# Kernel tuning notes

Measured on AMD Instinct MI355X. Metric: run time of the kernel, lower is better.

## Reference

```python
import jax, jax.numpy as jnp
import numpy as np

L = 2048          # seq len
DIM = 1024        # model dim
NL = 12           # num layers
VOCAB = 50257
PAD_VOCAB = 50264 # vocab padded to multiple of 8 for embedding
N = 16            # ssm state dim
K = 4             # conv kernel size
E = 2048          # d_inner = expand * dim
DTR = 64          # dt_rank = ceil(dim/16)
EPS = 1e-5


def setup_inputs() -> dict:
    key = jax.random.key(0)
    ks = jax.random.split(key, 12)
    s = 0.02
    f32 = jnp.float32
    # HiPPO-style A init: A_log = log(1..N) broadcast over channels
    A_log = jnp.log(jnp.broadcast_to(jnp.arange(1, N + 1, dtype=f32), (NL, E, N)))
    return {
        "input_ids": jax.random.randint(ks[0], (L,), 0, VOCAB),
        "embed": jax.random.normal(ks[1], (PAD_VOCAB, DIM), f32) * s,
        "in_proj_w": jax.random.normal(ks[2], (NL, 2 * E, DIM), f32) * s,
        "conv_w": jax.random.normal(ks[3], (NL, E, K), f32) * s,
        "conv_b": jnp.zeros((NL, E), f32),
        "x_proj_w": jax.random.normal(ks[4], (NL, DTR + 2 * N, E), f32) * s,
        "dt_proj_w": jax.random.normal(ks[5], (NL, E, DTR), f32) * s,
        "dt_proj_b": jax.random.normal(ks[6], (NL, E), f32) * 0.1,
        "A_log": A_log,
        "D_param": jnp.ones((NL, E), f32),
        "out_proj_w": jax.random.normal(ks[7], (NL, DIM, E), f32) * s,
        "norm_w": jnp.ones((NL, DIM), f32),
        "norm_f_w": jnp.ones((DIM,), f32),
        "head_w": jax.random.normal(ks[8], (VOCAB, DIM), f32) * s,
    }


def rmsnorm(x, w):
    # per-token RMSNorm over last axis (matches eqx.nn.RMSNorm vmapped per token)
    inv = jax.lax.rsqrt(jnp.mean(x * x, axis=-1, keepdims=True) + EPS)
    return x * inv * w


def causal_dw_conv(x, w, b):
    # x: [L, E], w: [E, K] depthwise causal conv, b: [E]
    out = jax.lax.conv_general_dilated(
        x.T[None],            # [1, E, L]
        w[:, None, :],        # [E, 1, K]
        (1,), [(K - 1, 0)],
        feature_group_count=E,
        dimension_numbers=("NCH", "OIH", "NCH"),
    )
    return out[0].T + b       # [L, E]


def mamba_block(x, in_w, cw, cb, xp_w, dt_w, dt_b, A_log, D, out_w):
    # x: [L, DIM]
    xz = x @ in_w.T                       # [L, 2E]
    xi, z = xz[:, :E], xz[:, E:]
    xc = jax.nn.silu(causal_dw_conv(xi, cw, cb))   # [L, E]
    dbc = xc @ xp_w.T                     # [L, DTR + 2N]
    dt = jax.nn.softplus(dbc[:, :DTR] @ dt_w.T + dt_b)  # [L, E]
    B = dbc[:, DTR:DTR + N]               # [L, N]
    C = dbc[:, DTR + N:]                  # [L, N]
    A = -jnp.exp(A_log)                   # [E, N]
    dA = jnp.exp(dt[:, :, None] * A)                       # [L, E, N]
    dBu = dt[:, :, None] * B[:, None, :] * xc[:, :, None]  # [L, E, N]

    def step(h, inp):
        dA_t, dBu_t = inp
        h = dA_t * h + dBu_t
        return h, h

    _, hs = jax.lax.scan(step, jnp.zeros((E, N), x.dtype), (dA, dBu))
    y = jnp.einsum("len,ln->le", hs, C) + D * xc
    y = y * jax.nn.silu(z)
    return y @ out_w.T                    # [L, DIM]


def reference(input_ids, embed, in_proj_w, conv_w, conv_b, x_proj_w,
              dt_proj_w, dt_proj_b, A_log, D_param, out_proj_w,
              norm_w, norm_f_w, head_w):
    x = embed[input_ids]                  # [L, DIM]
    res = None
    for i in range(NL):
        res = x + res if res is not None else x
        h = rmsnorm(res, norm_w[i])
        x = mamba_block(h, in_proj_w[i], conv_w[i], conv_b[i], x_proj_w[i],
                        dt_proj_w[i], dt_proj_b[i], A_log[i], D_param[i],
                        out_proj_w[i])
    res = x + res
    x = rmsnorm(res, norm_f_w)
    return x @ head_w.T                   # [L, VOCAB]
```

## Files before the change

kernel.cpp:

```cpp
#include <hip/hip_runtime.h>
#include <math.h>

#define LSEQ 2048
#define DMODEL 1024
#define NLAYER 12
#define NVOCAB 50257
#define NPADV 50304
#define EDIM 2048
#define NST 16
#define DTRANK 64
#define EPSV 1e-5f
#define NCHUNK 64
#define TCHUNK 32

typedef __attribute__((ext_vector_type(4))) float float4v;
typedef __attribute__((ext_vector_type(8))) short short8v;
typedef __attribute__((ext_vector_type(4))) unsigned short ushort4v;
typedef unsigned short u16;

__device__ __forceinline__ u16 f2bf(float f) {
    union { float f; unsigned int u; } v; v.f = f;
    unsigned int r = v.u + 0x7FFFu + ((v.u >> 16) & 1u);
    return (u16)(r >> 16);
}

__device__ __forceinline__ ushort4v cvt4(float4 a) {
    ushort4v r; r[0] = f2bf(a.x); r[1] = f2bf(a.y); r[2] = f2bf(a.z); r[3] = f2bf(a.w);
    return r;
}

__device__ __forceinline__ short8v pack8(float4 a, float4 b) {
    short8v r;
    r[0] = (short)f2bf(a.x); r[1] = (short)f2bf(a.y); r[2] = (short)f2bf(a.z); r[3] = (short)f2bf(a.w);
    r[4] = (short)f2bf(b.x); r[5] = (short)f2bf(b.y); r[6] = (short)f2bf(b.z); r[7] = (short)f2bf(b.w);
    return r;
}

__device__ __forceinline__ float4v mfma_bf16(short8v a, short8v b, float4v c) {
    return __builtin_amdgcn_mfma_f32_16x16x32_bf16(a, b, c, 0, 0, 0);
}

__device__ __forceinline__ void gload_lds16(const void* g, void* l) {
    __builtin_amdgcn_global_load_lds(
        (const __attribute__((address_space(1))) unsigned int*)g,
        (__attribute__((address_space(3))) unsigned int*)l,
        16, 0, 0);
}

__global__ __launch_bounds__(256) void k_embed(const int* __restrict__ ids,
                                               const float* __restrict__ emb,
                                               float* __restrict__ res) {
    const int t = blockIdx.x;
    const int row = ids[t];
    ((float4*)(res + (size_t)t * DMODEL))[threadIdx.x] =
        ((const float4*)(emb + (size_t)row * DMODEL))[threadIdx.x];
}

template<bool ADD>
__global__ __launch_bounds__(256) void k_addnorm(float* __restrict__ res,
                                                 const float* __restrict__ xin,
                                                 const float* __restrict__ w,
                                                 u16* __restrict__ h) {
    const int t = blockIdx.x;
    const int i = threadIdx.x;
    float4 r = ((float4*)(res + (size_t)t * DMODEL))[i];
    if (ADD) {
        float4 xv = ((const float4*)(xin + (size_t)t * DMODEL))[i];
        r.x += xv.x; r.y += xv.y; r.z += xv.z; r.w += xv.w;
        ((float4*)(res + (size_t)t * DMODEL))[i] = r;
    }
    float ss = r.x * r.x + r.y * r.y + r.z * r.z + r.w * r.w;
#pragma unroll
    for (int off = 32; off > 0; off >>= 1) ss += __shfl_xor(ss, off);
    __shared__ float part[4];
    if ((i & 63) == 0) part[i >> 6] = ss;
    __syncthreads();
    float tot = part[0] + part[1] + part[2] + part[3];
    const float inv = rsqrtf(tot * (1.f / DMODEL) + EPSV);
    float4 wv = ((const float4*)w)[i];
    float4 o;
    o.x = r.x * inv * wv.x; o.y = r.y * inv * wv.y;
    o.z = r.z * inv * wv.z; o.w = r.w * inv * wv.w;
    ((ushort4v*)(h + (size_t)t * DMODEL))[i] = cvt4(o);
}

__global__ __launch_bounds__(256) void k_cvt(const float* __restrict__ s, u16* __restrict__ d,
                                             long long n, long long ntot) {
    const long long stride = (long long)gridDim.x * 256 * 8;
    for (long long i = ((long long)blockIdx.x * 256 + threadIdx.x) * 8; i < ntot; i += stride) {
        ushort4v lo, hi;
        if (i < n) {
            float4 a = *(const float4*)(s + i);
            float4 b = *(const float4*)(s + i + 4);
            lo = cvt4(a); hi = cvt4(b);
        } else {
            lo[0] = lo[1] = lo[2] = lo[3] = 0;
            hi[0] = hi[1] = hi[2] = hi[3] = 0;
        }
        *(ushort4v*)(d + i) = lo;
        *(ushort4v*)(d + i + 4) = hi;
    }
}

__global__ __launch_bounds__(256) void k_cvt2(const float* __restrict__ sa, u16* __restrict__ da, long long na,
                                              const float* __restrict__ sb, u16* __restrict__ db, long long nb) {
    const long long tot = na + nb;
    const long long stride = (long long)gridDim.x * 256 * 8;
    for (long long i = ((long long)blockIdx.x * 256 + threadIdx.x) * 8; i < tot; i += stride) {
        const float* s; u16* d; long long o;
        if (i < na) { s = sa; d = da; o = i; } else { s = sb; d = db; o = i - na; }
        float4 a = *(const float4*)(s + o);
        float4 b = *(const float4*)(s + o + 4);
        *(ushort4v*)(d + o) = cvt4(a);
        *(ushort4v*)(d + o + 4) = cvt4(b);
    }
}

template<int TM, int TN>
__global__ __launch_bounds__(256) void k_gemm_bf(const u16* __restrict__ A,
                                                 const u16* __restrict__ W,
                                                 float* __restrict__ C,
                                                 int N, int K, int ldc) {
    constexpr int NI = TM / 32, NJ = TN / 32, CA = TM / 64, CB = TN / 64;
    __shared__ u16 As[TM * 32];
    __shared__ u16 Bs[TN * 32];
    const int tid = threadIdx.x;
    const int lane = tid & 63;
    const int wave = tid >> 6;
    const int l16 = lane & 15;
    const int quad = lane >> 4;
    const int wm = (wave >> 1) * (TM / 2);
    const int wn = (wave & 1) * (TN / 2);
    const int srow = lane >> 2;
    const int scol = (lane & 3) * 8;
    const int bm = blockIdx.x, bn = blockIdx.y;

    const u16* Ab = A + ((size_t)bm * TM + srow) * K + scol;
    const u16* Wb = W + ((size_t)bn * TN + srow) * K + scol;

    float4v acc[NI][NJ];
#pragma unroll
    for (int i = 0; i < NI; ++i)
#pragma unroll
        for (int j = 0; j < NJ; ++j)
#pragma unroll
            for (int r = 0; r < 4; ++r) acc[i][j][r] = 0.f;

    for (int k0 = 0; k0 < K; k0 += 32) {
#pragma unroll
        for (int c = 0; c < CA; ++c) {
            const int chunk = wave * CA + c;
            gload_lds16(Ab + (size_t)chunk * 16 * K + k0, &As[chunk * 512]);
        }
#pragma unroll
        for (int c = 0; c < CB; ++c) {
            const int chunk = wave * CB + c;
            gload_lds16(Wb + (size_t)chunk * 16 * K + k0, &Bs[chunk * 512]);
        }
        __syncthreads();
        short8v af[NI], bfr[NJ];
#pragma unroll
        for (int i = 0; i < NI; ++i)
            af[i] = *(const short8v*)&As[(wm + i * 16 + l16) * 32 + quad * 8];
#pragma unroll
        for (int j = 0; j < NJ; ++j)
            bfr[j] = *(const short8v*)&Bs[(wn + j * 16 + l16) * 32 + quad * 8];
#pragma unroll
        for (int i = 0; i < NI; ++i)
#pragma unroll
            for (int j = 0; j < NJ; ++j)
                acc[i][j] = mfma_bf16(af[i], bfr[j], acc[i][j]);
        __syncthreads();
    }

#pragma unroll
    for (int i = 0; i < NI; ++i) {
        const int row0 = bm * TM + wm + i * 16 + quad * 4;
#pragma unroll
        for (int j = 0; j < NJ; ++j) {
            const int col = bn * TN + wn + j * 16 + l16;
            if (col < N) {
#pragma unroll
                for (int r = 0; r < 4; ++r)
                    C[(size_t)(row0 + r) * ldc + col] = acc[i][j][r];
            }
        }
    }
}

template<int EPI>
__global__ __launch_bounds__(256) void k_gemm(const float* __restrict__ A,
                                              const float* __restrict__ W,
                                              float* __restrict__ C,
                                              const float* __restrict__ bias,
                                              int N, int K, int lda, int ldw, int ldc) {
    __shared__ u16 As[128][32];
    __shared__ u16 Bs[128][32];
    const int tid = threadIdx.x;
    const int lane = tid & 63;
    const int wave = tid >> 6;
    const int l16 = lane & 15;
    const int quad = lane >> 4;
    const int wm = (wave >> 1) * 64;
    const int wn = (wave & 1) * 64;
    const int srow = tid >> 3;
    const int scol = (tid & 7) * 4;
    const int bm = blockIdx.x, bn = blockIdx.y;

    const float* Ap = A + (size_t)(bm * 128 + srow) * lda + scol;
    const int gn0 = bn * 128 + srow;

    float4 apf[4], bpf[4];
#pragma unroll
    for (int i = 0; i < 4; ++i) {
        apf[i] = *(const float4*)(Ap + (size_t)(32 * i) * lda);
        const int gn = gn0 + 32 * i;
        bpf[i] = (gn < N) ? *(const float4*)(W + (size_t)gn * ldw + scol)
                          : make_float4(0.f, 0.f, 0.f, 0.f);
    }

    float4v acc[4][4];
#pragma unroll
    for (int i = 0; i < 4; ++i)
#pragma unroll
        for (int j = 0; j < 4; ++j)
#pragma unroll
            for (int r = 0; r < 4; ++r) acc[i][j][r] = 0.f;

    int k0 = 0;
    while (true) {
#pragma unroll
        for (int i = 0; i < 4; ++i) {
            *(ushort4v*)&As[srow + 32 * i][scol] = cvt4(apf[i]);
            *(ushort4v*)&Bs[srow + 32 * i][scol] = cvt4(bpf[i]);
        }
        __syncthreads();
        k0 += 32;
        const bool more = (k0 < K);
        if (more) {
#pragma unroll
            for (int i = 0; i < 4; ++i) {
                apf[i] = *(const float4*)(Ap + (size_t)(32 * i) * lda + k0);
                const int gn = gn0 + 32 * i;
                bpf[i] = (gn < N) ? *(const float4*)(W + (size_t)gn * ldw + scol + k0)
                                  : make_float4(0.f, 0.f, 0.f, 0.f);
            }
        }
        short8v af[4], bfr[4];
#pragma unroll
        for (int i = 0; i < 4; ++i)
            af[i] = *(const short8v*)&As[wm + i * 16 + l16][quad * 8];
#pragma unroll
        for (int j = 0; j < 4; ++j)
            bfr[j] = *(const short8v*)&Bs[wn + j * 16 + l16][quad * 8];
#pragma unroll
        for (int i = 0; i < 4; ++i)
#pragma unroll
            for (int j = 0; j < 4; ++j)
                acc[i][j] = mfma_bf16(af[i], bfr[j], acc[i][j]);
        if (!more) break;
        __syncthreads();
    }

#pragma unroll
    for (int i = 0; i < 4; ++i) {
        const int row0 = bm * 128 + wm + i * 16 + quad * 4;
#pragma unroll
        for (int j = 0; j < 4; ++j) {
            const int col = bn * 128 + wn + j * 16 + l16;
            if (col < N) {
#pragma unroll
                for (int r = 0; r < 4; ++r) {
                    float v = acc[i][j][r];
                    if (EPI == 1) {
                        v += bias[col];
                        v = (v > 20.f) ? v : log1pf(__expf(v));
                    }
                    C[(size_t)(row0 + r) * ldc + col] = v;
                }
            }
        }
    }
}

__global__ __launch_bounds__(256) void k_conv(const float* __restrict__ xz,
                                              const float* __restrict__ cw,
                                              const float* __restrict__ cb,
                                              float* __restrict__ xc) {
    const int e = blockIdx.x * 256 + threadIdx.x;
    const int t0 = blockIdx.y * 8;
    const float w0 = cw[e * 4 + 0], w1 = cw[e * 4 + 1], w2 = cw[e * 4 + 2], w3 = cw[e * 4 + 3];
    const float b = cb[e];
    float xm3 = (t0 >= 3) ? xz[(size_t)(t0 - 3) * (2 * EDIM) + e] : 0.f;
    float xm2 = (t0 >= 2) ? xz[(size_t)(t0 - 2) * (2 * EDIM) + e] : 0.f;
    float xm1 = (t0 >= 1) ? xz[(size_t)(t0 - 1) * (2 * EDIM) + e] : 0.f;
#pragma unroll
    for (int s = 0; s < 8; ++s) {
        const int t = t0 + s;
        const float xt = xz[(size_t)t * (2 * EDIM) + e];
        const float v = w0 * xm3 + w1 * xm2 + w2 * xm1 + w3 * xt + b;
        xc[(size_t)t * EDIM + e] = v / (1.f + __expf(-v));
        xm3 = xm2; xm2 = xm1; xm1 = xt;
    }
}

__global__ __launch_bounds__(256) void k_xproj(const float* __restrict__ xc,
                                               const float* __restrict__ W,
                                               float* __restrict__ dbc) {
    const int tid = threadIdx.x;
    const int wave = tid >> 6, lane = tid & 63;
    const int l16 = lane & 15, quad = lane >> 4;
    const int m = blockIdx.x * 16 + l16;
    const int kb = wave * (EDIM / 4);
    float4v acc[6];
#pragma unroll
    for (int j = 0; j < 6; ++j)
#pragma unroll
        for (int r = 0; r < 4; ++r) acc[j][r] = 0.f;

    for (int ks = 0; ks < EDIM / 4; ks += 32) {
        const int k = kb + ks + quad * 8;
        const float* ap = xc + (size_t)m * EDIM + k;
        const short8v af = pack8(*(const float4*)ap, *(const float4*)(ap + 4));
#pragma unroll
        for (int j = 0; j < 6; ++j) {
            const float* wp = W + (size_t)(j * 16 + l16) * EDIM + k;
            const short8v bf = pack8(*(const float4*)wp, *(const float4*)(wp + 4));
            acc[j] = mfma_bf16(af, bf, acc[j]);
        }
    }
    __shared__ float red[4][16][96];
#pragma unroll
    for (int j = 0; j < 6; ++j)
#pragma unroll
        for (int r = 0; r < 4; ++r)
            red[wave][quad * 4 + r][j * 16 + l16] = acc[j][r];
    __syncthreads();
    for (int idx = tid; idx < 16 * 96; idx += 256) {
        const int r = idx / 96, c = idx % 96;
        const float s = red[0][r][c] + red[1][r][c] + red[2][r][c] + red[3][r][c];
        dbc[(size_t)(blockIdx.x * 16 + r) * 96 + c] = s;
    }
}

__global__ __launch_bounds__(256) void k_scanA(const float* __restrict__ dt,
                                               const float* __restrict__ xc,
                                               const float* __restrict__ dbc,
                                               const float* __restrict__ Al,
                                               float* __restrict__ hpart,
                                               float* __restrict__ sdtb) {
    const int e = blockIdx.y * 256 + threadIdx.x;
    const int c = blockIdx.x;
    float a[NST];
#pragma unroll
    for (int n = 0; n < NST; ++n) a[n] = -__expf(Al[(size_t)e * NST + n]);
    bool fast = true;
#pragma unroll
    for (int n = 0; n < NST; ++n)
        fast = fast && (fabsf(a[n] + (float)(n + 1)) < 1e-3f * (float)(n + 1));
    __align__(16) float h[NST];
#pragma unroll
    for (int n = 0; n < NST; ++n) h[n] = 0.f;
    float sdt = 0.f;
    const int t0 = c * TCHUNK;
    if (fast) {
        for (int s = 0; s < TCHUNK; ++s) {
            const int t = t0 + s;
            const float d = dt[(size_t)t * EDIM + e];
            const float x = xc[(size_t)t * EDIM + e];
            __align__(16) float Bv[NST];
#pragma unroll
            for (int q = 0; q < 4; ++q)
                *(float4*)&Bv[q * 4] = *(const float4*)&dbc[(size_t)t * 96 + 64 + q * 4];
            const float u = d * x;
            sdt += d;
            const float d1 = __expf(-d);
            float pw = 1.f;
#pragma unroll
            for (int n = 0; n < NST; ++n) { pw *= d1; h[n] = fmaf(pw, h[n], u * Bv[n]); }
        }
    } else {
        for (int s = 0; s < TCHUNK; ++s) {
            const int t = t0 + s;
            const float d = dt[(size_t)t * EDIM + e];
            const float x = xc[(size_t)t * EDIM + e];
            __align__(16) float Bv[NST];
#pragma unroll
            for (int q = 0; q < 4; ++q)
                *(float4*)&Bv[q * 4] = *(const float4*)&dbc[(size_t)t * 96 + 64 + q * 4];
            const float u = d * x;
            sdt += d;
#pragma unroll
            for (int n = 0; n < NST; ++n) h[n] = fmaf(__expf(d * a[n]), h[n], u * Bv[n]);
        }
    }
#pragma unroll
    for (int n = 0; n < NST; n += 4)
        *(float4*)&hpart[((size_t)c * EDIM + e) * NST + n] = *(float4*)&h[n];
    sdtb[(size_t)c * EDIM + e] = sdt;
}

__global__ __launch_bounds__(256) void k_scanB(float* __restrict__ hio,
                                               const float* __restrict__ sdtb,
                                               const float* __restrict__ Al) {
    const int idx = blockIdx.x * 256 + threadIdx.x;
    const int e = idx >> 4;
    const float a = -__expf(Al[idx]);
    float carry = 0.f;
    for (int c = 0; c < NCHUNK; ++c) {
        const size_t off = ((size_t)c * EDIM + e) * NST + (idx & 15);
        const float hp = hio[off];
        const float ap = __expf(a * sdtb[(size_t)c * EDIM + e]);
        hio[off] = carry;
        carry = fmaf(ap, carry, hp);
    }
}

__global__ __launch_bounds__(256) void k_scanC(const float* __restrict__ dt,
                                               const float* __restrict__ xc,
                                               const float* __restrict__ dbc,
                                               const float* __restrict__ xz,
                                               const float* __restrict__ Al,
                                               const float* __restrict__ Dl,
                                               const float* __restrict__ hin,
                                               u16* __restrict__ y) {
    const int e = blockIdx.y * 256 + threadIdx.x;
    const int c = blockIdx.x;
    float a[NST];
#pragma unroll
    for (int n = 0; n < NST; ++n) a[n] = -__expf(Al[(size_t)e * NST + n]);
    bool fast = true;
#pragma unroll
    for (int n = 0; n < NST; ++n)
        fast = fast && (fabsf(a[n] + (float)(n + 1)) < 1e-3f * (float)(n + 1));
    __align__(16) float h[NST];
#pragma unroll
    for (int n = 0; n < NST; n += 4)
        *(float4*)&h[n] = *(const float4*)&hin[((size_t)c * EDIM + e) * NST + n];
    const float Dv = Dl[e];
    const int t0 = c * TCHUNK;
    for (int s = 0; s < TCHUNK; ++s) {
        const int t = t0 + s;
        const float d = dt[(size_t)t * EDIM + e];
        const float x = xc[(size_t)t * EDIM + e];
        __align__(16) float Bv[NST], Cv[NST];
#pragma unroll
        for (int q = 0; q < 4; ++q) {
            *(float4*)&Bv[q * 4] = *(const float4*)&dbc[(size_t)t * 96 + 64 + q * 4];
            *(float4*)&Cv[q * 4] = *(const float4*)&dbc[(size_t)t * 96 + 80 + q * 4];
        }
        const float u = d * x;
        float ys = 0.f;
        if (fast) {
            const float d1 = __expf(-d);
            float pw = 1.f;
#pragma unroll
            for (int n = 0; n < NST; ++n) {
                pw *= d1;
                h[n] = fmaf(pw, h[n], u * Bv[n]);
                ys = fmaf(h[n], Cv[n], ys);
            }
        } else {
#pragma unroll
            for (int n = 0; n < NST; ++n) {
                h[n] = fmaf(__expf(d * a[n]), h[n], u * Bv[n]);
                ys = fmaf(h[n], Cv[n], ys);
            }
        }
        const float z = xz[(size_t)t * (2 * EDIM) + EDIM + e];
        const float yv = ys + Dv * x;
        y[(size_t)t * EDIM + e] = f2bf(yv * (z / (1.f + __expf(-z))));
    }
}

extern "C" void kernel_launch(void* const* d_in, const int* in_sizes, int n_in,
                              void* d_out, int out_size, void* d_ws, size_t ws_size,
                              hipStream_t stream) {
    const int*   ids   = (const int*)d_in[0];
    const float* emb   = (const float*)d_in[1];
    const float* inW   = (const float*)d_in[2];
    const float* convW = (const float*)d_in[3];
    const float* convB = (const float*)d_in[4];
    const float* xpW   = (const float*)d_in[5];
    const float* dtW   = (const float*)d_in[6];
    const float* dtB   = (const float*)d_in[7];
    const float* Alog  = (const float*)d_in[8];
    const float* Dpar  = (const float*)d_in[9];
    const float* outW  = (const float*)d_in[10];
    const float* normW = (const float*)d_in[11];
    const float* normF = (const float*)d_in[12];
    const float* headW = (const float*)d_in[13];
    float* out = (float*)d_out;

    float* ws    = (float*)d_ws;
    float* res   = ws;
    float* xzb   = res   + (size_t)LSEQ * DMODEL;
    float* xcb   = xzb   + (size_t)LSEQ * 2 * EDIM;
    float* dbcb  = xcb   + (size_t)LSEQ * EDIM;
    float* dtb   = dbcb  + (size_t)LSEQ * 96;
    float* xob   = dtb   + (size_t)LSEQ * EDIM;
    float* hpart = xob   + (size_t)LSEQ * DMODEL;
    float* sdtb  = hpart + (size_t)NCHUNK * EDIM * NST;
    u16* hbf  = (u16*)(sdtb + (size_t)NCHUNK * EDIM);
    u16* ybf  = hbf  + (size_t)LSEQ * DMODEL;
    u16* wbf  = ybf  + (size_t)LSEQ * EDIM;
    u16* wbf2 = wbf  + (size_t)2 * EDIM * DMODEL;

    k_embed<<<LSEQ, 256, 0, stream>>>(ids, emb, res);

    for (int i = 0; i < NLAYER; ++i) {
        if (i == 0)
            k_addnorm<false><<<LSEQ, 256, 0, stream>>>(res, nullptr, normW, hbf);
        else
            k_addnorm<true><<<LSEQ, 256, 0, stream>>>(res, xob, normW + (size_t)i * DMODEL, hbf);

        k_cvt2<<<4096, 256, 0, stream>>>(inW + (size_t)i * 2 * EDIM * DMODEL, wbf,
                                         (long long)2 * EDIM * DMODEL,
                                         outW + (size_t)i * DMODEL * EDIM, wbf2,
                                         (long long)DMODEL * EDIM);

        k_gemm_bf<128, 128><<<dim3(16, 32), 256, 0, stream>>>(hbf, wbf, xzb,
                2 * EDIM, DMODEL, 2 * EDIM);

        k_conv<<<dim3(8, 256), 256, 0, stream>>>(xzb, convW + (size_t)i * EDIM * 4,
                convB + (size_t)i * EDIM, xcb);

        k_xproj<<<128, 256, 0, stream>>>(xcb, xpW + (size_t)i * 96 * EDIM, dbcb);

        k_gemm<1><<<dim3(16, 16), 256, 0, stream>>>(dbcb, dtW + (size_t)i * EDIM * DTRANK,
                dtb, dtB + (size_t)i * EDIM, EDIM, DTRANK, 96, DTRANK, EDIM);

        const float* Al = Alog + (size_t)i * EDIM * NST;
        k_scanA<<<dim3(NCHUNK, EDIM / 256), 256, 0, stream>>>(dtb, xcb, dbcb, Al, hpart, sdtb);
        k_scanB<<<(EDIM * NST) / 256, 256, 0, stream>>>(hpart, sdtb, Al);
        k_scanC<<<dim3(NCHUNK, EDIM / 256), 256, 0, stream>>>(dtb, xcb, dbcb, xzb, Al,
                Dpar + (size_t)i * EDIM, hpart, ybf);

        k_gemm_bf<64, 64><<<dim3(32, 16), 256, 0, stream>>>(ybf, wbf2, xob,
                DMODEL, EDIM, DMODEL);
    }

    k_addnorm<true><<<LSEQ, 256, 0, stream>>>(res, xob, normF, hbf);

    k_cvt<<<4096, 256, 0, stream>>>(headW, wbf,
            (long long)NVOCAB * DMODEL, (long long)NPADV * DMODEL);
    k_gemm_bf<128, 128><<<dim3(16, NPADV / 128), 256, 0, stream>>>(hbf, wbf, out,
            NVOCAB, DMODEL, NVOCAB);
}
```

Baseline: 3.261 ms.

## Add 256x256-tile double-buffered bf16 GEMM for in_proj and LM head

```diff
diff --git a/kernel.cpp b/kernel.cpp
--- a/kernel.cpp
+++ b/kernel.cpp
@@ -5,7 +5,7 @@
 #define DMODEL 1024
 #define NLAYER 12
 #define NVOCAB 50257
-#define NPADV 50304
+#define NPADV 50432
 #define EDIM 2048
 #define NST 16
 #define DTRANK 64
@@ -113,6 +113,115 @@
         float4 b = *(const float4*)(s + o + 4);
         *(ushort4v*)(d + o) = cvt4(a);
         *(ushort4v*)(d + o + 4) = cvt4(b);
+    }
+}
+
+template<int MT>
+__global__ __launch_bounds__(512, 2) void k_gemm256(const u16* __restrict__ A,
+                                                    const u16* __restrict__ W,
+                                                    float* __restrict__ C,
+                                                    int N, int K, int ldc, int cpx) {
+    __shared__ __align__(128) u16 lds[2][2][2][8192];
+    const int tid = threadIdx.x;
+    const int w = tid >> 6;
+    const int lane = tid & 63;
+    const int l16 = lane & 15;
+    const int quad = lane >> 4;
+    const int wm = (w >> 2) * 128;
+    const int wn = (w & 3) * 64;
+    const int ha = w >> 2;
+    const int hb = (w >> 1) & 1;
+    const int bid = blockIdx.x;
+    const int orig = (bid & 7) * cpx + (bid >> 3);
+    const int bm = orig & (MT - 1);
+    const int bn = orig / MT;
+    const int row0 = bm * 256, col0 = bn * 256;
+
+    int srow[2], scol[2];
+#pragma unroll
+    for (int q = 0; q < 2; ++q) {
+        int off = q * 8192 + w * 1024 + lane * 16;
+        off ^= ((off >> 9) & 1) << 5;
+        srow[q] = off >> 7;
+        scol[q] = (off & 127) >> 1;
+    }
+    const int qx = (quad * 16) ^ (((l16 >> 2) & 1) << 5);
+    const int bA = l16 * 128 + qx;
+    const int bB = ((wn & 127) + l16) * 128 + qx;
+
+    float4v acc[8][4];
+#pragma unroll
+    for (int i = 0; i < 8; ++i)
+#pragma unroll
+        for (int j = 0; j < 4; ++j)
+#pragma unroll
+            for (int r = 0; r < 4; ++r) acc[i][j][r] = 0.f;
+
+    const int NT = K >> 6;
+
+    auto stage_tile = [&](int buf, int t) {
+#pragma unroll
+        for (int h = 0; h < 2; ++h)
+#pragma unroll
+            for (int q = 0; q < 2; ++q) {
+                gload_lds16(A + (size_t)(row0 + h * 128 + srow[q]) * K + t * 64 + scol[q],
+                            &lds[buf][0][h][q * 4096 + w * 512]);
+                gload_lds16(W + (size_t)(col0 + h * 128 + srow[q]) * K + t * 64 + scol[q],
+                            &lds[buf][1][h][q * 4096 + w * 512]);
+            }
+    };
+
+    stage_tile(0, 0);
+    stage_tile(1, 1);
+    asm volatile("s_waitcnt vmcnt(8)" ::: "memory");
+    __builtin_amdgcn_s_barrier();
+
+    for (int n = 0; n < NT; ++n) {
+        const u16* As0 = &lds[n & 1][0][ha][0];
+        const u16* Bs0 = &lds[n & 1][1][hb][0];
+#pragma unroll
+        for (int ph = 0; ph < 4; ++ph) {
+            const int ih = ph & 1;
+            const int ks = ph >> 1;
+            short8v af[4], bf[4];
+#pragma unroll
+            for (int ii = 0; ii < 4; ++ii)
+                af[ii] = *(const short8v*)((const char*)As0 + (bA + ih * 8192 + ii * 2048 + ks * 64));
+#pragma unroll
+            for (int j = 0; j < 4; ++j)
+                bf[j] = *(const short8v*)((const char*)Bs0 + (bB + j * 2048 + ks * 64));
+            __builtin_amdgcn_s_barrier();
+            __builtin_amdgcn_s_setprio(1);
+#pragma unroll
+            for (int ii = 0; ii < 4; ++ii)
+#pragma unroll
+                for (int j = 0; j < 4; ++j)
+                    acc[ih * 4 + ii][j] = mfma_bf16(af[ii], bf[j], acc[ih * 4 + ii][j]);
+            __builtin_amdgcn_s_setprio(0);
+            if (ph == 3) {
+                if (n + 2 < NT) {
+                    stage_tile(n & 1, n + 2);
+                    asm volatile("s_waitcnt vmcnt(8)" ::: "memory");
+                } else if (n < NT - 1) {
+                    asm volatile("s_waitcnt vmcnt(0)" ::: "memory");
+                }
+            }
+            __builtin_amdgcn_s_barrier();
+        }
+    }
+
+#pragma unroll
+    for (int i = 0; i < 8; ++i) {
+        const int row = row0 + wm + i * 16 + quad * 4;
+#pragma unroll
+        for (int j = 0; j < 4; ++j) {
+            const int col = col0 + wn + j * 16 + l16;
+            if (col < N) {
+#pragma unroll
+                for (int r = 0; r < 4; ++r)
+                    C[(size_t)(row + r) * ldc + col] = acc[i][j][r];
+            }
+        }
     }
 }
 
@@ -519,8 +628,8 @@
                                          outW + (size_t)i * DMODEL * EDIM, wbf2,
                                          (long long)DMODEL * EDIM);
 
-        k_gemm_bf<128, 128><<<dim3(16, 32), 256, 0, stream>>>(hbf, wbf, xzb,
-                2 * EDIM, DMODEL, 2 * EDIM);
+        k_gemm256<8><<<dim3(128), 512, 0, stream>>>(hbf, wbf, xzb,
+                2 * EDIM, DMODEL, 2 * EDIM, 16);
 
         k_conv<<<dim3(8, 256), 256, 0, stream>>>(xzb, convW + (size_t)i * EDIM * 4,
                 convB + (size_t)i * EDIM, xcb);
@@ -544,6 +653,6 @@
 
     k_cvt<<<4096, 256, 0, stream>>>(headW, wbf,
             (long long)NVOCAB * DMODEL, (long long)NPADV * DMODEL);
-    k_gemm_bf<128, 128><<<dim3(16, NPADV / 128), 256, 0, stream>>>(hbf, wbf, out,
-            NVOCAB, DMODEL, NVOCAB);
-}
+    k_gemm256<8><<<dim3(8 * (NPADV / 256)), 512, 0, stream>>>(hbf, wbf, out,
+            NVOCAB, DMODEL, NVOCAB, NPADV / 256);
+}
```

New measurement: 3.392 ms. 4.0% more time.
